# Performance work log

Hardware: AMD Instinct MI355X
Metric: run time of the kernel (lower is better)

The kernel has to match this reference:

```python
import jax, jax.numpy as jnp
import numpy as np

K = 3  # kernel size
PAD = K // 2


def setup_inputs() -> dict:
    key = jax.random.key(0)
    k1, k2, k3 = jax.random.split(key, 3)
    B, C, H, W = 8, 192, 128, 128
    x = jax.random.normal(k1, (B, C, H, W), dtype=jnp.float32)
    kernel = 0.02 * jax.random.normal(k2, (C, K * K), dtype=jnp.float32)
    gate_w = 0.02 * jax.random.normal(k3, (C,), dtype=jnp.float32)
    gate_b = jnp.zeros((C,), dtype=jnp.float32)
    return {"x": x, "kernel": kernel, "gate_w": gate_w, "gate_b": gate_b}


def reference(x, kernel, gate_w, gate_b):
    B, C, H, W = x.shape
    # F.unfold with zero padding: patches[b,c,ki*K+kj,h,w] = x_pad[b,c,h+ki,w+kj]
    xp = jnp.pad(x, ((0, 0), (0, 0), (PAD, PAD), (PAD, PAD)))
    patches = jnp.stack(
        [xp[:, :, i:i + H, j:j + W] for i in range(K) for j in range(K)],
        axis=2,
    )  # [B, C, K*K, H, W]
    # depthwise 1x1 gate: per-channel scale + bias, then sigmoid
    theta = jax.nn.sigmoid(x * gate_w[None, :, None, None] + gate_b[None, :, None, None])
    # max-plus: max_v [ f(u-v) + theta(u) * k(v) ]
    scored = patches + theta[:, :, None] * kernel[None, :, :, None, None]
    return jnp.max(scored, axis=2)  # [B, C, H, W]
```

## Files before the change

kernel.cpp:

```cpp
#include <hip/hip_runtime.h>
#include <math.h>

#define BB 8
#define CC 192
#define HH 128
#define WW 128
#define TILE_H 16
#define LDS_ROWS (TILE_H + 2)
#define LDS_COLS (WW + 2)

__global__ __launch_bounds__(256) void dynmorph_kernel(
    const float* __restrict__ x,
    const float* __restrict__ kern,
    const float* __restrict__ gw,
    const float* __restrict__ gb,
    float* __restrict__ out)
{
    __shared__ float s[LDS_ROWS][LDS_COLS];

    const int tid = threadIdx.x;
    const int h0  = blockIdx.x * TILE_H;
    const int c   = blockIdx.y;
    const int b   = blockIdx.z;

    const float* xp = x   + ((size_t)(b * CC + c)) * (HH * WW);
    float*       op = out + ((size_t)(b * CC + c)) * (HH * WW);

    if (tid < LDS_ROWS) {
        s[tid][0]      = 0.0f;
        s[tid][WW + 1] = 0.0f;
    }

    for (int i = tid; i < LDS_ROWS * (WW / 4); i += 256) {
        const int lr = i >> 5;
        const int vc = i & 31;
        const int g  = h0 - 1 + lr;
        float4 v;
        if (g >= 0 && g < HH) {
            v = *(const float4*)(xp + g * WW + vc * 4);
        } else {
            v = make_float4(0.0f, 0.0f, 0.0f, 0.0f);
        }
        const int col = 1 + vc * 4;
        s[lr][col + 0] = v.x;
        s[lr][col + 1] = v.y;
        s[lr][col + 2] = v.z;
        s[lr][col + 3] = v.w;
    }

    const float k0 = kern[c * 9 + 0];
    const float k1 = kern[c * 9 + 1];
    const float k2 = kern[c * 9 + 2];
    const float k3 = kern[c * 9 + 3];
    const float k4 = kern[c * 9 + 4];
    const float k5 = kern[c * 9 + 5];
    const float k6 = kern[c * 9 + 6];
    const float k7 = kern[c * 9 + 7];
    const float k8 = kern[c * 9 + 8];
    const float gwc = gw[c];
    const float gbc = gb[c];

    __syncthreads();

    for (int i = tid; i < TILE_H * WW; i += 256) {
        const int r = i >> 7;
        const int w = i & 127;

        const float center = s[r + 1][w + 1];
        const float t      = fmaf(center, gwc, gbc);
        const float theta  = 1.0f / (1.0f + __expf(-t));

        float m;
        m = fmaf(theta, k0, s[r + 0][w + 0]);
        m = fmaxf(m, fmaf(theta, k1, s[r + 0][w + 1]));
        m = fmaxf(m, fmaf(theta, k2, s[r + 0][w + 2]));
        m = fmaxf(m, fmaf(theta, k3, s[r + 1][w + 0]));
        m = fmaxf(m, fmaf(theta, k4, center));
        m = fmaxf(m, fmaf(theta, k5, s[r + 1][w + 2]));
        m = fmaxf(m, fmaf(theta, k6, s[r + 2][w + 0]));
        m = fmaxf(m, fmaf(theta, k7, s[r + 2][w + 1]));
        m = fmaxf(m, fmaf(theta, k8, s[r + 2][w + 2]));

        op[(h0 + r) * WW + w] = m;
    }
}

extern "C" void kernel_launch(void* const* d_in, const int* in_sizes, int n_in,
                              void* d_out, int out_size, void* d_ws, size_t ws_size,
                              hipStream_t stream) {
    const float* x    = (const float*)d_in[0];
    const float* kern = (const float*)d_in[1];
    const float* gw   = (const float*)d_in[2];
    const float* gb   = (const float*)d_in[3];
    float* out        = (float*)d_out;

    dim3 grid(HH / TILE_H, CC, BB);
    dim3 block(256);
    dynmorph_kernel<<<grid, block, 0, stream>>>(x, kern, gw, gb, out);
}
```

Before: 185.2 us.

## Replace LDS tiling with register sliding window and wavefront shuffles

```diff
diff --git a/kernel.cpp b/kernel.cpp
--- a/kernel.cpp
+++ b/kernel.cpp
@@ -5,9 +5,43 @@
 #define CC 192
 #define HH 128
 #define WW 128
-#define TILE_H 16
-#define LDS_ROWS (TILE_H + 2)
-#define LDS_COLS (WW + 2)
+#define RPT 16
+
+struct RowReg { float l; float4 v; float r; };
+
+__device__ __forceinline__ RowReg load_row(const float* __restrict__ xp,
+                                           int g, int col, int wg) {
+    float4 v;
+    if (g >= 0 && g < HH) {
+        v = *(const float4*)(xp + g * WW + col);
+    } else {
+        v = make_float4(0.0f, 0.0f, 0.0f, 0.0f);
+    }
+    float l = __shfl_up(v.w, 1);
+    float r = __shfl_down(v.x, 1);
+    RowReg rr;
+    rr.l = (wg == 0)  ? 0.0f : l;
+    rr.r = (wg == 31) ? 0.0f : r;
+    rr.v = v;
+    return rr;
+}
+
+__device__ __forceinline__ float col9(float a0, float a1, float a2,
+                                      float b0, float b1, float b2,
+                                      float c0, float c1, float c2,
+                                      float th, const float* kk) {
+    float m;
+    m = fmaf(th, kk[0], a0);
+    m = fmaxf(m, fmaf(th, kk[1], a1));
+    m = fmaxf(m, fmaf(th, kk[2], a2));
+    m = fmaxf(m, fmaf(th, kk[3], b0));
+    m = fmaxf(m, fmaf(th, kk[4], b1));
+    m = fmaxf(m, fmaf(th, kk[5], b2));
+    m = fmaxf(m, fmaf(th, kk[6], c0));
+    m = fmaxf(m, fmaf(th, kk[7], c1));
+    m = fmaxf(m, fmaf(th, kk[8], c2));
+    return m;
+}
 
 __global__ __launch_bounds__(256) void dynmorph_kernel(
     const float* __restrict__ x,
@@ -16,72 +50,56 @@
     const float* __restrict__ gb,
     float* __restrict__ out)
 {
-    __shared__ float s[LDS_ROWS][LDS_COLS];
+    const int tid  = threadIdx.x;
+    const int lane = tid & 63;
+    const int wg   = lane & 31;
+    const int rs   = (tid >> 6) * 2 + (lane >> 5);
+    const int col  = wg * 4;
+    const int r0   = rs * RPT;
 
-    const int tid = threadIdx.x;
-    const int h0  = blockIdx.x * TILE_H;
-    const int c   = blockIdx.y;
-    const int b   = blockIdx.z;
+    const int bc = blockIdx.x;
+    const int c  = bc % CC;
 
-    const float* xp = x   + ((size_t)(b * CC + c)) * (HH * WW);
-    float*       op = out + ((size_t)(b * CC + c)) * (HH * WW);
+    const float* xp = x   + (size_t)bc * (HH * WW);
+    float*       op = out + (size_t)bc * (HH * WW);
 
-    if (tid < LDS_ROWS) {
-        s[tid][0]      = 0.0f;
-        s[tid][WW + 1] = 0.0f;
-    }
-
-    for (int i = tid; i < LDS_ROWS * (WW / 4); i += 256) {
-        const int lr = i >> 5;
-        const int vc = i & 31;
-        const int g  = h0 - 1 + lr;
-        float4 v;
-        if (g >= 0 && g < HH) {
-            v = *(const float4*)(xp + g * WW + vc * 4);
-        } else {
-            v = make_float4(0.0f, 0.0f, 0.0f, 0.0f);
-        }
-        const int col = 1 + vc * 4;
-        s[lr][col + 0] = v.x;
-        s[lr][col + 1] = v.y;
-        s[lr][col + 2] = v.z;
-        s[lr][col + 3] = v.w;
-    }
-
-    const float k0 = kern[c * 9 + 0];
-    const float k1 = kern[c * 9 + 1];
-    const float k2 = kern[c * 9 + 2];
-    const float k3 = kern[c * 9 + 3];
-    const float k4 = kern[c * 9 + 4];
-    const float k5 = kern[c * 9 + 5];
-    const float k6 = kern[c * 9 + 6];
-    const float k7 = kern[c * 9 + 7];
-    const float k8 = kern[c * 9 + 8];
+    float kk[9];
+#pragma unroll
+    for (int i = 0; i < 9; ++i) kk[i] = kern[c * 9 + i];
     const float gwc = gw[c];
     const float gbc = gb[c];
 
-    __syncthreads();
+    RowReg A = load_row(xp, r0 - 1, col, wg);
+    RowReg B = load_row(xp, r0,     col, wg);
 
-    for (int i = tid; i < TILE_H * WW; i += 256) {
-        const int r = i >> 7;
-        const int w = i & 127;
+#pragma unroll 4
+    for (int g = 0; g < RPT; ++g) {
+        const int gr = r0 + g;
+        RowReg C = load_row(xp, gr + 1, col, wg);
 
-        const float center = s[r + 1][w + 1];
-        const float t      = fmaf(center, gwc, gbc);
-        const float theta  = 1.0f / (1.0f + __expf(-t));
+        float t0 = 1.0f / (1.0f + __expf(-fmaf(B.v.x, gwc, gbc)));
+        float t1 = 1.0f / (1.0f + __expf(-fmaf(B.v.y, gwc, gbc)));
+        float t2 = 1.0f / (1.0f + __expf(-fmaf(B.v.z, gwc, gbc)));
+        float t3 = 1.0f / (1.0f + __expf(-fmaf(B.v.w, gwc, gbc)));
 
-        float m;
-        m = fmaf(theta, k0, s[r + 0][w + 0]);
-        m = fmaxf(m, fmaf(theta, k1, s[r + 0][w + 1]));
-        m = fmaxf(m, fmaf(theta, k2, s[r + 0][w + 2]));
-        m = fmaxf(m, fmaf(theta, k3, s[r + 1][w + 0]));
-        m = fmaxf(m, fmaf(theta, k4, center));
-        m = fmaxf(m, fmaf(theta, k5, s[r + 1][w + 2]));
-        m = fmaxf(m, fmaf(theta, k6, s[r + 2][w + 0]));
-        m = fmaxf(m, fmaf(theta, k7, s[r + 2][w + 1]));
-        m = fmaxf(m, fmaf(theta, k8, s[r + 2][w + 2]));
+        float4 o;
+        o.x = col9(A.l,   A.v.x, A.v.y,
+                   B.l,   B.v.x, B.v.y,
+                   C.l,   C.v.x, C.v.y, t0, kk);
+        o.y = col9(A.v.x, A.v.y, A.v.z,
+                   B.v.x, B.v.y, B.v.z,
+                   C.v.x, C.v.y, C.v.z, t1, kk);
+        o.z = col9(A.v.y, A.v.z, A.v.w,
+                   B.v.y, B.v.z, B.v.w,
+                   C.v.y, C.v.z, C.v.w, t2, kk);
+        o.w = col9(A.v.z, A.v.w, A.r,
+                   B.v.z, B.v.w, B.r,
+                   C.v.z, C.v.w, C.r,   t3, kk);
 
-        op[(h0 + r) * WW + w] = m;
+        *(float4*)(op + gr * WW + col) = o;
+
+        A = B;
+        B = C;
     }
 }
 
@@ -94,7 +112,7 @@
     const float* gb   = (const float*)d_in[3];
     float* out        = (float*)d_out;
 
-    dim3 grid(HH / TILE_H, CC, BB);
+    dim3 grid(BB * CC);
     dim3 block(256);
     dynmorph_kernel<<<grid, block, 0, stream>>>(x, kern, gw, gb, out);
 }
```

Result: no change. 185.9 us (+0.4%).
